# Performance work log

Hardware: AMD Instinct MI355X
Metric: run time of the kernel (lower is better)

The kernel has to match this reference:

```python
import jax, jax.numpy as jnp
import numpy as np

B, T, C, H = 2, 2048, 1024, 16
HD = C // H  # head dim = 64


def setup_inputs() -> dict:
    key = jax.random.key(0)
    ks = jax.random.split(key, 5)
    s = 1.0 / np.sqrt(C)
    return {
        "x": jax.random.normal(ks[0], (B, T, C), dtype=jnp.float32),
        "W_attn": jax.random.normal(ks[1], (3 * C, C), dtype=jnp.float32) * s,
        "b_attn": jax.random.normal(ks[2], (3 * C,), dtype=jnp.float32) * 0.02,
        "W_proj": jax.random.normal(ks[3], (C, C), dtype=jnp.float32) * s,
        "b_proj": jax.random.normal(ks[4], (C,), dtype=jnp.float32) * 0.02,
    }


def reference(x, W_attn, b_attn, W_proj, b_proj):
    Bx, Tx, Cx = x.shape
    # fused QKV projection (torch Linear: x @ W.T + b)
    qkv = x @ W_attn.T + b_attn                      # [B,T,3C]
    q, k, v = jnp.split(qkv, 3, axis=-1)
    # [B,T,C] -> [B,H,T,hd]
    q = q.reshape(Bx, Tx, H, HD).transpose(0, 2, 1, 3)
    k = k.reshape(Bx, Tx, H, HD).transpose(0, 2, 1, 3)
    v = v.reshape(Bx, Tx, H, HD).transpose(0, 2, 1, 3)
    scale = 1.0 / np.sqrt(HD)
    att = jnp.einsum('bhqd,bhkd->bhqk', q, k) * scale  # [B,H,T,T]
    causal = jnp.tril(jnp.ones((Tx, Tx), dtype=bool))
    att = jnp.where(causal[None, None], att, -jnp.inf)
    att = jax.nn.softmax(att, axis=-1)
    y = jnp.einsum('bhqk,bhkd->bhqd', att, v)          # [B,H,T,hd]
    y = y.transpose(0, 2, 1, 3).reshape(Bx, Tx, Cx)
    return y @ W_proj.T + b_proj
```

## Files before the change

### kernel.cpp

```cpp
#include <hip/hip_runtime.h>

typedef unsigned short ushort_t;
typedef __bf16 bf16x8 __attribute__((ext_vector_type(8)));
typedef float f32x4 __attribute__((ext_vector_type(4)));

__device__ inline ushort_t f2bf(float f) {
  unsigned int u = __builtin_bit_cast(unsigned int, f);
  u += 0x7fff + ((u >> 16) & 1);
  return (ushort_t)(u >> 16);
}

__device__ inline unsigned pk_bf(float a, float b) {
  unsigned ua = __builtin_bit_cast(unsigned, a);
  unsigned ub = __builtin_bit_cast(unsigned, b);
  ua += 0x7fff + ((ua >> 16) & 1);
  ub += 0x7fff + ((ub >> 16) & 1);
  return __builtin_amdgcn_perm(ub, ua, 0x07060302);
}

__device__ inline void async_ld16(const ushort_t* g, const ushort_t* l) {
  __builtin_amdgcn_global_load_lds(
      (const __attribute__((address_space(1))) void*)g,
      (__attribute__((address_space(3))) void*)l, 16, 0, 0);
}

template <int IMM>
__device__ inline void waitcnt_barrier() {
  asm volatile("" ::: "memory");
  __builtin_amdgcn_s_waitcnt(IMM);
  __builtin_amdgcn_s_barrier();
  asm volatile("" ::: "memory");
}

__global__ void cvt_all(const float* __restrict__ x, const float* __restrict__ wa,
                        const float* __restrict__ wp, ushort_t* __restrict__ xb,
                        ushort_t* __restrict__ wab, ushort_t* __restrict__ wpb) {
  int i = blockIdx.x * 256 + threadIdx.x;
  const float* src;
  ushort_t* dst;
  int off;
  if (i < 1048576) { src = x; dst = xb; off = i; }
  else if (i < 1835008) { src = wa; dst = wab; off = i - 1048576; }
  else { src = wp; dst = wpb; off = i - 1835008; }
  float4 f = ((const float4*)src)[off];
  unsigned long long p = (unsigned long long)f2bf(f.x)
      | ((unsigned long long)f2bf(f.y) << 16)
      | ((unsigned long long)f2bf(f.z) << 32)
      | ((unsigned long long)f2bf(f.w) << 48);
  ((unsigned long long*)dst)[off] = p;
}

template <int BM, int BN, int IM, int JN, int MODE, int TPB>
__global__ __launch_bounds__(TPB) void gemm_bt(
    const ushort_t* __restrict__ A, const ushort_t* __restrict__ B,
    const float* __restrict__ bias, float* __restrict__ Cf,
    ushort_t* __restrict__ Cb, ushort_t* __restrict__ vtb,
    int M, int N, int K, int ldc, float qscale) {
  constexpr int NWN = BN / (JN * 16);
  constexpr int NL = (BM + BN) * 32 / (TPB * 8);
  constexpr int WIMM = 0x0F70 | NL;
  __shared__ __align__(16) ushort_t As[3][BM * 32];
  __shared__ __align__(16) ushort_t Bs[3][BN * 32];
  const int tid = threadIdx.x;
  const int wave = tid >> 6, lane = tid & 63;
  const int quad = lane >> 4, l16 = lane & 15;
  const int wr = wave / NWN, wc = wave % NWN;
  const int wm = wr * IM * 16, wn = wc * JN * 16;
  const int m0 = blockIdx.y * BM, n0 = blockIdx.x * BN;
  const ushort_t* Ag = A + (size_t)m0 * K;
  const ushort_t* Bg = B + (size_t)n0 * K;
  const int slot = (quad ^ ((l16 >> 1) & 3)) * 8;
  f32x4 acc[IM][JN] = {};

  auto stage = [&](int kt, int bsel) {
    int k0 = kt * 32;
#pragma unroll
    for (int p = 0; p < BM * 4 / TPB; ++p) {
      int ci = p * TPB + tid;
      int row = ci >> 2, ch = (ci & 3) ^ ((ci >> 3) & 3);
      async_ld16(Ag + (size_t)row * K + k0 + ch * 8, As[bsel] + (p * TPB + wave * 64) * 8);
    }
#pragma unroll
    for (int p = 0; p < BN * 4 / TPB; ++p) {
      int ci = p * TPB + tid;
      int row = ci >> 2, ch = (ci & 3) ^ ((ci >> 3) & 3);
      async_ld16(Bg + (size_t)row * K + k0 + ch * 8, Bs[bsel] + (p * TPB + wave * 64) * 8);
    }
  };

  const int KT = K / 32;
  stage(0, 0);
  stage(1, 1);
  for (int kt = 0; kt < KT; ++kt) {
    waitcnt_barrier<WIMM>();
    if (kt + 2 < KT) stage(kt + 2, (kt + 2) % 3);
    const ushort_t* Ac = As[kt % 3];
    const ushort_t* Bc = Bs[kt % 3];
    bf16x8 af[IM], bfr[JN];
#pragma unroll
    for (int i = 0; i < IM; ++i)
      af[i] = *(const bf16x8*)(Ac + (wm + i * 16 + l16) * 32 + slot);
#pragma unroll
    for (int j = 0; j < JN; ++j)
      bfr[j] = *(const bf16x8*)(Bc + (wn + j * 16 + l16) * 32 + slot);
#pragma unroll
    for (int i = 0; i < IM; ++i)
#pragma unroll
      for (int j = 0; j < JN; ++j)
        acc[i][j] = __builtin_amdgcn_mfma_f32_16x16x32_bf16(af[i], bfr[j], acc[i][j], 0, 0, 0);
  }

  if (MODE == 1 && n0 >= 2048) {
#pragma unroll
    for (int j = 0; j < JN; ++j) {
      int col = n0 + wn + j * 16 + l16;
      int cv = col - 2048;
      float bv = bias[col];
      size_t rowbase = ((size_t)(cv >> 6)) * 64 + (cv & 63);
#pragma unroll
      for (int i = 0; i < IM; ++i) {
        int rowb = m0 + wm + i * 16 + quad * 4;
        int bb = rowb >> 11, t = rowb & 2047;
        uint2 pp;
        pp.x = pk_bf(acc[i][j][0] + bv, acc[i][j][1] + bv);
        pp.y = pk_bf(acc[i][j][2] + bv, acc[i][j][3] + bv);
        *(uint2*)(vtb + (((size_t)bb * 1024 + rowbase) * 2048 + t)) = pp;
      }
    }
    return;
  }
#pragma unroll
  for (int j = 0; j < JN; ++j) {
    int col = n0 + wn + j * 16 + l16;
    float bv = bias[col];
    float sc = (MODE == 1 && col < 1024) ? qscale : 1.0f;
#pragma unroll
    for (int i = 0; i < IM; ++i)
#pragma unroll
      for (int r = 0; r < 4; ++r) {
        int row = m0 + wm + i * 16 + quad * 4 + r;
        float v = (acc[i][j][r] + bv) * sc;
        if (MODE == 1)
          Cb[(size_t)row * ldc + col] = f2bf(v);
        else
          Cf[(size_t)row * ldc + col] = v;
      }
  }
}

__global__ __launch_bounds__(256, 3) void flash5(
    const ushort_t* __restrict__ qk, const ushort_t* __restrict__ vt,
    ushort_t* __restrict__ y, float* __restrict__ ob0, float* __restrict__ ob1,
    float* __restrict__ lb0, float* __restrict__ lb1) {
  __shared__ __align__(16) ushort_t Kb[2][4096];
  __shared__ __align__(16) ushort_t Vb[2][4096];
  __shared__ __align__(16) ushort_t Ps[4][1152];
  const int tid = threadIdx.x, wave = tid >> 6, lane = tid & 63;
  const int quad = lane >> 4, l16 = lane & 15;
  const int r7 = l16 & 7;
  const int x = blockIdx.x, bh = blockIdx.y;
  const int b = bh >> 4, h = bh & 15;
  const int bT = b * 2048;
  int qt, klo, khi, mode;
  if (x < 16)      { qt = 31 - x;        klo = 0;            khi = (qt + 2) / 2; mode = 1; }
  else if (x < 32) { qt = 31 - (x - 16); klo = (qt + 2) / 2; khi = qt + 1;       mode = 2; }
  else             { qt = 47 - x;        klo = 0;            khi = qt + 1;       mode = 0; }
  ushort_t* Pw = Ps[wave];

  const ushort_t* qrow = qk + (size_t)(bT + qt * 64 + wave * 16 + l16) * 2048 + h * 64 + quad * 8;
  bf16x8 qf[2];
  qf[0] = *(const bf16x8*)(qrow);
  qf[1] = *(const bf16x8*)(qrow + 32);

  auto stage = [&](int kt, int bsel) {
    int k0 = kt * 64;
#pragma unroll
    for (int i = 0; i < 2; ++i) {
      int ci = i * 256 + tid;
      int row = ci >> 3, ch = (ci & 7) ^ (row & 7);
      async_ld16(qk + (size_t)(bT + k0 + row) * 2048 + 1024 + h * 64 + ch * 8,
                 Kb[bsel] + (i * 256 + wave * 64) * 8);
      async_ld16(vt + (size_t)(bh * 64 + row) * 2048 + k0 + ch * 8,
                 Vb[bsel] + (i * 256 + wave * 64) * 8);
    }
  };

  f32x4 o[4] = {};
  float l = 0.f;

  stage(klo, 0);
  for (int kt = klo; kt < khi; ++kt) {
    const int cur = (kt - klo) & 1;
    waitcnt_barrier<0x0F70>();
    if (kt + 1 < khi) stage(kt + 1, cur ^ 1);
    const ushort_t* Kc = Kb[cur];
    const ushort_t* Vc = Vb[cur];
    f32x4 s[4] = {};
#pragma unroll
    for (int ks = 0; ks < 2; ++ks)
#pragma unroll
      for (int j = 0; j < 4; ++j) {
        bf16x8 kf = *(const bf16x8*)(Kc + (j * 16 + l16) * 64 + (((ks * 4 + quad) ^ r7) * 8));
        s[j] = __builtin_amdgcn_mfma_f32_16x16x32_bf16(kf, qf[ks], s[j], 0, 0, 0);
      }
    if (kt == qt) {
      int qloc = wave * 16 + l16;
#pragma unroll
      for (int j = 0; j < 4; ++j)
#pragma unroll
        for (int r = 0; r < 4; ++r)
          if (j * 16 + quad * 4 + r > qloc) s[j][r] = -1e30f;
    }
#pragma unroll
    for (int j = 0; j < 4; ++j) {
#pragma unroll
      for (int r = 0; r < 4; ++r) {
        float pv = exp2f(s[j][r]);
        s[j][r] = pv;
        l += pv;
      }
      uint2 pp;
      pp.x = pk_bf(s[j][0], s[j][1]);
      pp.y = pk_bf(s[j][2], s[j][3]);
      *(uint2*)(Pw + l16 * 72 + j * 16 + quad * 4) = pp;
    }
    __builtin_amdgcn_s_waitcnt(0xc07f);
    bf16x8 pf[2];
    pf[0] = *(const bf16x8*)(Pw + l16 * 72 + quad * 8);
    pf[1] = *(const bf16x8*)(Pw + l16 * 72 + 32 + quad * 8);
#pragma unroll
    for (int ks = 0; ks < 2; ++ks)
#pragma unroll
      for (int j = 0; j < 4; ++j) {
        bf16x8 vf = *(const bf16x8*)(Vc + (j * 16 + l16) * 64 + (((ks * 4 + quad) ^ r7) * 8));
        o[j] = __builtin_amdgcn_mfma_f32_16x16x32_bf16(vf, pf[ks], o[j], 0, 0, 0);
      }
  }

  l += __shfl_xor(l, 16, 64);
  l += __shfl_xor(l, 32, 64);
  if (mode == 0) {
    float inv = 1.f / l;
    size_t row = (size_t)(bT + qt * 64 + wave * 16 + l16);
#pragma unroll
    for (int j = 0; j < 4; ++j) {
      uint2 pp;
      pp.x = pk_bf(o[j][0] * inv, o[j][1] * inv);
      pp.y = pk_bf(o[j][2] * inv, o[j][3] * inv);
      *(uint2*)(y + row * 1024 + h * 64 + j * 16 + quad * 4) = pp;
    }
  } else {
    float* ob = (mode == 1) ? ob0 : ob1;
    float* lb = (mode == 1) ? lb0 : lb1;
    size_t base = (((size_t)bh * 16 + (qt - 16)) * 64 + wave * 16 + l16) * 64;
#pragma unroll
    for (int j = 0; j < 4; ++j)
      *(f32x4*)(ob + base + j * 16 + quad * 4) = o[j];
    if (quad == 0)
      lb[((size_t)bh * 16 + (qt - 16)) * 64 + wave * 16 + l16] = l;
  }
}

__global__ void combine(const float* __restrict__ ob0, const float* __restrict__ ob1,
                        const float* __restrict__ lb0, const float* __restrict__ lb1,
                        ushort_t* __restrict__ y) {
  int id = blockIdx.x * 256 + threadIdx.x;
  int dg = id & 15, q = (id >> 4) & 63, qx = (id >> 10) & 15, bh = id >> 14;
  size_t po = (((size_t)bh * 16 + qx) * 64 + q) * 64 + dg * 4;
  float4 a = *(const float4*)(ob0 + po);
  float4 c = *(const float4*)(ob1 + po);
  size_t pl = ((size_t)bh * 16 + qx) * 64 + q;
  float inv = 1.f / (lb0[pl] + lb1[pl]);
  uint2 pp;
  pp.x = pk_bf((a.x + c.x) * inv, (a.y + c.y) * inv);
  pp.y = pk_bf((a.z + c.z) * inv, (a.w + c.w) * inv);
  size_t row = (size_t)((bh >> 4) * 2048 + (16 + qx) * 64 + q);
  *(uint2*)(y + row * 1024 + (bh & 15) * 64 + dg * 4) = pp;
}

extern "C" void kernel_launch(void* const* d_in, const int* in_sizes, int n_in,
                              void* d_out, int out_size, void* d_ws, size_t ws_size,
                              hipStream_t stream) {
  const float* x  = (const float*)d_in[0];
  const float* Wa = (const float*)d_in[1];
  const float* ba = (const float*)d_in[2];
  const float* Wp = (const float*)d_in[3];
  const float* bp = (const float*)d_in[4];
  float* out = (float*)d_out;
  char* ws = (char*)d_ws;
  ushort_t* xb  = (ushort_t*)(ws);
  ushort_t* Wab = (ushort_t*)(ws + 8388608);
  ushort_t* Wpb = (ushort_t*)(ws + 14680064);
  ushort_t* qkb = (ushort_t*)(ws + 16777216);
  ushort_t* yb  = (ushort_t*)(ws + 33554432);
  ushort_t* vtb = (ushort_t*)(ws + 41943040);
  float* ob0 = (float*)d_out;
  float* ob1 = (float*)(ws);
  float* lb0 = (float*)(ws + 8388608);
  float* lb1 = (float*)(ws + 8519680);

  cvt_all<<<8192, 256, 0, stream>>>(x, Wa, Wp, xb, Wab, Wpb);
  gemm_bt<128, 128, 4, 2, 1, 512><<<dim3(24, 32), 512, 0, stream>>>(
      xb, Wab, ba, nullptr, qkb, vtb, 4096, 3072, 1024, 2048, 0.18033688011112042f);
  flash5<<<dim3(48, 32), 256, 0, stream>>>(qkb, vtb, yb, ob0, ob1, lb0, lb1);
  combine<<<2048, 256, 0, stream>>>(ob0, ob1, lb0, lb1, yb);
  gemm_bt<64, 64, 2, 2, 0, 256><<<dim3(16, 64), 256, 0, stream>>>(
      yb, Wpb, bp, out, nullptr, nullptr, 4096, 1024, 1024, 1024, 1.0f);
}
```

Measured before the change: 199.8 us.

## Use 128-row query tiles per block and drop split-K combine pass

The flash kernel now gives each wave 32 query rows instead of 16, so every block covers 128 queries. Each K and V tile loaded into shared memory is reused across twice as many queries, and the K fragments are hoisted into registers once per tile. The split-KV scheme with partial outputs and a separate combine kernel is removed, which saves one launch and the fp32 partial-result traffic. The grid drops to 512 blocks with uneven causal work per block, which risks load imbalance, lower occupancy and higher register pressure.

```diff
diff --git a/kernel.cpp b/kernel.cpp
--- a/kernel.cpp
+++ b/kernel.cpp
@@ -148,29 +148,29 @@
   }
 }
 
-__global__ __launch_bounds__(256, 3) void flash5(
+__global__ __launch_bounds__(256, 3) void flash6(
     const ushort_t* __restrict__ qk, const ushort_t* __restrict__ vt,
-    ushort_t* __restrict__ y, float* __restrict__ ob0, float* __restrict__ ob1,
-    float* __restrict__ lb0, float* __restrict__ lb1) {
+    ushort_t* __restrict__ y) {
   __shared__ __align__(16) ushort_t Kb[2][4096];
   __shared__ __align__(16) ushort_t Vb[2][4096];
-  __shared__ __align__(16) ushort_t Ps[4][1152];
+  __shared__ __align__(16) ushort_t Ps[4][32 * 72];
   const int tid = threadIdx.x, wave = tid >> 6, lane = tid & 63;
   const int quad = lane >> 4, l16 = lane & 15;
   const int r7 = l16 & 7;
-  const int x = blockIdx.x, bh = blockIdx.y;
+  const int xx = blockIdx.x, bh = blockIdx.y;
+  const int Q = (xx < 8) ? (15 - xx) : (xx - 8);
   const int b = bh >> 4, h = bh & 15;
   const int bT = b * 2048;
-  int qt, klo, khi, mode;
-  if (x < 16)      { qt = 31 - x;        klo = 0;            khi = (qt + 2) / 2; mode = 1; }
-  else if (x < 32) { qt = 31 - (x - 16); klo = (qt + 2) / 2; khi = qt + 1;       mode = 2; }
-  else             { qt = 47 - x;        klo = 0;            khi = qt + 1;       mode = 0; }
+  const int qw = Q * 128 + wave * 32;
   ushort_t* Pw = Ps[wave];
 
-  const ushort_t* qrow = qk + (size_t)(bT + qt * 64 + wave * 16 + l16) * 2048 + h * 64 + quad * 8;
-  bf16x8 qf[2];
-  qf[0] = *(const bf16x8*)(qrow);
-  qf[1] = *(const bf16x8*)(qrow + 32);
+  bf16x8 qf[2][2];
+#pragma unroll
+  for (int f = 0; f < 2; ++f) {
+    const ushort_t* qrow = qk + (size_t)(bT + qw + f * 16 + l16) * 2048 + h * 64 + quad * 8;
+    qf[f][0] = *(const bf16x8*)(qrow);
+    qf[f][1] = *(const bf16x8*)(qrow + 32);
+  }
 
   auto stage = [&](int kt, int bsel) {
     int k0 = kt * 64;
@@ -185,97 +185,89 @@
     }
   };
 
-  f32x4 o[4] = {};
-  float l = 0.f;
-
-  stage(klo, 0);
-  for (int kt = klo; kt < khi; ++kt) {
-    const int cur = (kt - klo) & 1;
+  f32x4 o[4][2] = {};
+  float lac[2] = {0.f, 0.f};
+  const int KT = 2 * Q + 2;
+
+  stage(0, 0);
+  for (int kt = 0; kt < KT; ++kt) {
+    const int cur = kt & 1;
     waitcnt_barrier<0x0F70>();
-    if (kt + 1 < khi) stage(kt + 1, cur ^ 1);
+    if (kt + 1 < KT) stage(kt + 1, cur ^ 1);
     const ushort_t* Kc = Kb[cur];
     const ushort_t* Vc = Vb[cur];
-    f32x4 s[4] = {};
+    bf16x8 kf[4][2];
+#pragma unroll
+    for (int j = 0; j < 4; ++j)
+#pragma unroll
+      for (int ks = 0; ks < 2; ++ks)
+        kf[j][ks] = *(const bf16x8*)(Kc + (j * 16 + l16) * 64 + (((ks * 4 + quad) ^ r7) * 8));
+    f32x4 s[4][2] = {};
 #pragma unroll
     for (int ks = 0; ks < 2; ++ks)
 #pragma unroll
       for (int j = 0; j < 4; ++j) {
-        bf16x8 kf = *(const bf16x8*)(Kc + (j * 16 + l16) * 64 + (((ks * 4 + quad) ^ r7) * 8));
-        s[j] = __builtin_amdgcn_mfma_f32_16x16x32_bf16(kf, qf[ks], s[j], 0, 0, 0);
-      }
-    if (kt == qt) {
-      int qloc = wave * 16 + l16;
-#pragma unroll
-      for (int j = 0; j < 4; ++j)
-#pragma unroll
-        for (int r = 0; r < 4; ++r)
-          if (j * 16 + quad * 4 + r > qloc) s[j][r] = -1e30f;
-    }
-#pragma unroll
-    for (int j = 0; j < 4; ++j) {
-#pragma unroll
-      for (int r = 0; r < 4; ++r) {
-        float pv = exp2f(s[j][r]);
-        s[j][r] = pv;
-        l += pv;
-      }
-      uint2 pp;
-      pp.x = pk_bf(s[j][0], s[j][1]);
-      pp.y = pk_bf(s[j][2], s[j][3]);
-      *(uint2*)(Pw + l16 * 72 + j * 16 + quad * 4) = pp;
-    }
+        s[j][0] = __builtin_amdgcn_mfma_f32_16x16x32_bf16(kf[j][ks], qf[0][ks], s[j][0], 0, 0, 0);
+        s[j][1] = __builtin_amdgcn_mfma_f32_16x16x32_bf16(kf[j][ks], qf[1][ks], s[j][1], 0, 0, 0);
+      }
+    if (kt >= KT - 2) {
+#pragma unroll
+      for (int f = 0; f < 2; ++f) {
+        int qloc = qw + f * 16 + l16;
+#pragma unroll
+        for (int j = 0; j < 4; ++j)
+#pragma unroll
+          for (int r = 0; r < 4; ++r)
+            if (kt * 64 + j * 16 + quad * 4 + r > qloc) s[j][f][r] = -1e30f;
+      }
+    }
+#pragma unroll
+    for (int f = 0; f < 2; ++f)
+#pragma unroll
+      for (int j = 0; j < 4; ++j) {
+#pragma unroll
+        for (int r = 0; r < 4; ++r) {
+          float pv = exp2f(s[j][f][r]);
+          s[j][f][r] = pv;
+          lac[f] += pv;
+        }
+        uint2 pp;
+        pp.x = pk_bf(s[j][f][0], s[j][f][1]);
+        pp.y = pk_bf(s[j][f][2], s[j][f][3]);
+        *(uint2*)(Pw + (f * 16 + l16) * 72 + j * 16 + quad * 4) = pp;
+      }
     __builtin_amdgcn_s_waitcnt(0xc07f);
-    bf16x8 pf[2];
-    pf[0] = *(const bf16x8*)(Pw + l16 * 72 + quad * 8);
-    pf[1] = *(const bf16x8*)(Pw + l16 * 72 + 32 + quad * 8);
+    bf16x8 pf[2][2];
+#pragma unroll
+    for (int ks = 0; ks < 2; ++ks)
+#pragma unroll
+      for (int f = 0; f < 2; ++f)
+        pf[ks][f] = *(const bf16x8*)(Pw + (f * 16 + l16) * 72 + ks * 32 + quad * 8);
 #pragma unroll
     for (int ks = 0; ks < 2; ++ks)
 #pragma unroll
       for (int j = 0; j < 4; ++j) {
         bf16x8 vf = *(const bf16x8*)(Vc + (j * 16 + l16) * 64 + (((ks * 4 + quad) ^ r7) * 8));
-        o[j] = __builtin_amdgcn_mfma_f32_16x16x32_bf16(vf, pf[ks], o[j], 0, 0, 0);
-      }
-  }
-
-  l += __shfl_xor(l, 16, 64);
-  l += __shfl_xor(l, 32, 64);
-  if (mode == 0) {
+        o[j][0] = __builtin_amdgcn_mfma_f32_16x16x32_bf16(vf, pf[ks][0], o[j][0], 0, 0, 0);
+        o[j][1] = __builtin_amdgcn_mfma_f32_16x16x32_bf16(vf, pf[ks][1], o[j][1], 0, 0, 0);
+      }
+  }
+
+#pragma unroll
+  for (int f = 0; f < 2; ++f) {
+    float l = lac[f];
+    l += __shfl_xor(l, 16, 64);
+    l += __shfl_xor(l, 32, 64);
     float inv = 1.f / l;
-    size_t row = (size_t)(bT + qt * 64 + wave * 16 + l16);
+    size_t row = (size_t)(bT + qw + f * 16 + l16);
 #pragma unroll
     for (int j = 0; j < 4; ++j) {
       uint2 pp;
-      pp.x = pk_bf(o[j][0] * inv, o[j][1] * inv);
-      pp.y = pk_bf(o[j][2] * inv, o[j][3] * inv);
+      pp.x = pk_bf(o[j][f][0] * inv, o[j][f][1] * inv);
+      pp.y = pk_bf(o[j][f][2] * inv, o[j][f][3] * inv);
       *(uint2*)(y + row * 1024 + h * 64 + j * 16 + quad * 4) = pp;
     }
-  } else {
-    float* ob = (mode == 1) ? ob0 : ob1;
-    float* lb = (mode == 1) ? lb0 : lb1;
-    size_t base = (((size_t)bh * 16 + (qt - 16)) * 64 + wave * 16 + l16) * 64;
-#pragma unroll
-    for (int j = 0; j < 4; ++j)
-      *(f32x4*)(ob + base + j * 16 + quad * 4) = o[j];
-    if (quad == 0)
-      lb[((size_t)bh * 16 + (qt - 16)) * 64 + wave * 16 + l16] = l;
-  }
-}
-
-__global__ void combine(const float* __restrict__ ob0, const float* __restrict__ ob1,
-                        const float* __restrict__ lb0, const float* __restrict__ lb1,
-                        ushort_t* __restrict__ y) {
-  int id = blockIdx.x * 256 + threadIdx.x;
-  int dg = id & 15, q = (id >> 4) & 63, qx = (id >> 10) & 15, bh = id >> 14;
-  size_t po = (((size_t)bh * 16 + qx) * 64 + q) * 64 + dg * 4;
-  float4 a = *(const float4*)(ob0 + po);
-  float4 c = *(const float4*)(ob1 + po);
-  size_t pl = ((size_t)bh * 16 + qx) * 64 + q;
-  float inv = 1.f / (lb0[pl] + lb1[pl]);
-  uint2 pp;
-  pp.x = pk_bf((a.x + c.x) * inv, (a.y + c.y) * inv);
-  pp.y = pk_bf((a.z + c.z) * inv, (a.w + c.w) * inv);
-  size_t row = (size_t)((bh >> 4) * 2048 + (16 + qx) * 64 + q);
-  *(uint2*)(y + row * 1024 + (bh & 15) * 64 + dg * 4) = pp;
+  }
 }
 
 extern "C" void kernel_launch(void* const* d_in, const int* in_sizes, int n_in,
@@ -294,16 +286,11 @@
   ushort_t* qkb = (ushort_t*)(ws + 16777216);
   ushort_t* yb  = (ushort_t*)(ws + 33554432);
   ushort_t* vtb = (ushort_t*)(ws + 41943040);
-  float* ob0 = (float*)d_out;
-  float* ob1 = (float*)(ws);
-  float* lb0 = (float*)(ws + 8388608);
-  float* lb1 = (float*)(ws + 8519680);
 
   cvt_all<<<8192, 256, 0, stream>>>(x, Wa, Wp, xb, Wab, Wpb);
   gemm_bt<128, 128, 4, 2, 1, 512><<<dim3(24, 32), 512, 0, stream>>>(
       xb, Wab, ba, nullptr, qkb, vtb, 4096, 3072, 1024, 2048, 0.18033688011112042f);
-  flash5<<<dim3(48, 32), 256, 0, stream>>>(qkb, vtb, yb, ob0, ob1, lb0, lb1);
-  combine<<<2048, 256, 0, stream>>>(ob0, ob1, lb0, lb1, yb);
+  flash6<<<dim3(16, 32), 256, 0, stream>>>(qkb, vtb, yb);
   gemm_bt<64, 64, 2, 2, 0, 256><<<dim3(16, 64), 256, 0, stream>>>(
       yb, Wpb, bp, out, nullptr, nullptr, 4096, 1024, 1024, 1024, 1.0f);
 }
```

New measurement: 210.2 us. 1.05x slower.
